# Performance work log

Measured on AMD Instinct MI355X. Metric: run time of the kernel, lower is better.

## Reference

```python
import jax, jax.numpy as jnp
import numpy as np

EPS = 1e-5
H = 8
N_BUCKETS = 32


def _instance_norm(x, gamma, beta):
    # x: [B, N, D]; torch InstanceNorm1d normalizes over the N (length) dim
    # per channel per batch element, using biased variance.
    m = jnp.mean(x, axis=1, keepdims=True)
    v = jnp.var(x, axis=1, keepdims=True)
    return (x - m) * jax.lax.rsqrt(v + EPS) * gamma + beta


def setup_inputs() -> dict:
    key = jax.random.key(0)
    ks = jax.random.split(key, 12)
    B, N, D, d_ff = 4, 512, 128, 512
    s = 1.0 / np.sqrt(D)
    sf = 1.0 / np.sqrt(d_ff)
    u = lambda k, shape, lim: jax.random.uniform(k, shape, jnp.float32, -lim, lim)
    return {
        "h": jax.random.normal(ks[0], (B, N, D), jnp.float32),
        "coords": jax.random.uniform(ks[1], (B, N, 2), jnp.float32),
        "W_Q": u(ks[2], (D, D), s),
        "W_K": u(ks[3], (D, D), s),
        "W_V": u(ks[4], (D, D), s),
        "W_O": u(ks[5], (D, D), s),
        "emb": jax.random.normal(ks[6], (N_BUCKETS, D), jnp.float32),  # n_heads*d_k == D
        "ffn_w1": u(ks[7], (D, d_ff), s),
        "ffn_b1": u(ks[8], (d_ff,), s),
        "ffn_w2": u(ks[9], (d_ff, D), sf),
        "ffn_b2": u(ks[10], (D,), sf),
        "gamma1": jnp.ones((D,), jnp.float32),
        "beta1": jnp.zeros((D,), jnp.float32),
        "gamma2": jnp.ones((D,), jnp.float32),
        "beta2": jnp.zeros((D,), jnp.float32),
    }


def reference(h, coords, W_Q, W_K, W_V, W_O, emb, ffn_w1, ffn_b1, ffn_w2,
              ffn_b2, gamma1, beta1, gamma2, beta2):
    B, N, D = h.shape
    Dk = D // H
    Q = (h @ W_Q).reshape(B, N, H, Dk)
    K = (h @ W_K).reshape(B, N, H, Dk)
    V = (h @ W_V).reshape(B, N, H, Dk)
    # content scores: [B, H, N, N]
    scores = jnp.einsum('bnhd,bmhd->bhnm', Q, K) / np.sqrt(Dk)
    # relative-distance bucket embeddings for all (i, j) pairs
    diff = coords[:, :, None, :] - coords[:, None, :, :]          # [B,N,N,2]
    dist = jax.lax.stop_gradient(jnp.sqrt(jnp.sum(diff * diff, -1)))
    buckets = jnp.clip((dist * N_BUCKETS).astype(jnp.int32), 0, N_BUCKETS - 1)
    r = emb[buckets].reshape(B, N, N, H, Dk)                      # [B,N,N,H,Dk]
    scores = scores + jnp.einsum('bnhd,bnmhd->bhnm', Q, r)
    attn = jax.nn.softmax(scores, axis=-1)
    h_attn = jnp.einsum('bhnm,bmhd->bnhd', attn, V).reshape(B, N, D) @ W_O
    h1 = _instance_norm(h + h_attn, gamma1, beta1)
    h_ffn = jax.nn.relu(h1 @ ffn_w1 + ffn_b1) @ ffn_w2 + ffn_b2
    return _instance_norm(h1 + h_ffn, gamma2, beta2)
```

## Files before the change

kernel.cpp:

```cpp
#include <hip/hip_runtime.h>
#include <hip/hip_bf16.h>

#define B_  4
#define N_  512
#define D_  128
#define H_  8
#define DK  16
#define DFF 512
#define NB  32
#define KS  4
#define FS  4

__global__ __launch_bounds__(256) void qkv_qe_kernel(
    const float* __restrict__ A,
    const float* __restrict__ WQ, const float* __restrict__ WK, const float* __restrict__ WV,
    const float* __restrict__ emb,
    float* __restrict__ Qo, float* __restrict__ Ko, float* __restrict__ Vo,
    float* __restrict__ QE)
{
    const float* Bw = blockIdx.z == 0 ? WQ : (blockIdx.z == 1 ? WK : WV);
    float*       C  = blockIdx.z == 0 ? Qo : (blockIdx.z == 1 ? Ko : Vo);
    const int wave = threadIdx.x >> 6;
    const int lane = threadIdx.x & 63;
    const int rbase = __builtin_amdgcn_readfirstlane((blockIdx.x * 4 + wave) * 2);
    const int col = lane * 2;

    float acc[2][2] = {};
#pragma unroll 2
    for (int k0 = 0; k0 < D_; k0 += 4) {
        float4 a0 = *(const float4*)&A[(size_t)(rbase + 0) * D_ + k0];
        float4 a1 = *(const float4*)&A[(size_t)(rbase + 1) * D_ + k0];
#pragma unroll
        for (int kk = 0; kk < 4; ++kk) {
            float2 bv = *(const float2*)&Bw[(size_t)(k0 + kk) * D_ + col];
            float x0 = (&a0.x)[kk], x1 = (&a1.x)[kk];
            acc[0][0] += x0 * bv.x; acc[0][1] += x0 * bv.y;
            acc[1][0] += x1 * bv.x; acc[1][1] += x1 * bv.y;
        }
    }
    *(float2*)&C[(size_t)(rbase + 0) * D_ + col] = make_float2(acc[0][0], acc[0][1]);
    *(float2*)&C[(size_t)(rbase + 1) * D_ + col] = make_float2(acc[1][0], acc[1][1]);

    if (blockIdx.z == 0) {
        __shared__ float Qls[8][132];
        *(float2*)&Qls[wave * 2 + 0][col] = make_float2(acc[0][0], acc[0][1]);
        *(float2*)&Qls[wave * 2 + 1][col] = make_float2(acc[1][0], acc[1][1]);
        __syncthreads();
        const int r  = threadIdx.x >> 5;
        const int hh = (threadIdx.x >> 2) & 7;
        const int k0 = (threadIdx.x & 3) * 8;
        const int grow = blockIdx.x * 8 + r;
        const float4* qv = (const float4*)&Qls[r][hh * DK];
        const float4 qa = qv[0], qb = qv[1], qc = qv[2], qd = qv[3];
        float* qe_out = QE + ((size_t)grow * H_ + hh) * NB + k0;
#pragma unroll 2
        for (int k = 0; k < 8; ++k) {
            const float4* ep = (const float4*)(emb + (size_t)(k0 + k) * D_ + hh * DK);
            float4 e0 = ep[0], e1 = ep[1], e2 = ep[2], e3 = ep[3];
            float d0 = fmaf(qa.x,e0.x, fmaf(qa.y,e0.y, fmaf(qa.z,e0.z, qa.w*e0.w)));
            float d1 = fmaf(qb.x,e1.x, fmaf(qb.y,e1.y, fmaf(qb.z,e1.z, qb.w*e1.w)));
            float d2 = fmaf(qc.x,e2.x, fmaf(qc.y,e2.y, fmaf(qc.z,e2.z, qc.w*e2.w)));
            float d3 = fmaf(qd.x,e3.x, fmaf(qd.y,e3.y, fmaf(qd.z,e3.z, qd.w*e3.w)));
            qe_out[k] = (d0 + d1) + (d2 + d3);
        }
    }
}

__global__ __launch_bounds__(256) void attn7_kernel(
    const float* __restrict__ Q, const float* __restrict__ K, const float* __restrict__ V,
    const float* __restrict__ QE, const float* __restrict__ coords,
    float* __restrict__ P)
{
    const int tid  = threadIdx.x;
    const int wave = tid >> 6;
    const int lane = tid & 63;
    const int bid  = blockIdx.x;
    const int ks    = bid & 3;
    const int chunk = (bid >> 2) & 7;
    const int h     = (bid >> 5) & (H_ - 1);
    const int b     = bid >> 8;
    const int row = b * N_ + chunk * 64 + lane;

    __shared__ float kl[64][16];
    __shared__ float vl[64][16];
    __shared__ float qel[64][NB + 1];
    __shared__ float ckrd[128][2];
    __shared__ float accl[4][64][17];

    const size_t hdbase = (size_t)b * N_ * D_ + h * DK;

    {
        int r = tid >> 2, part = tid & 3;
        const float* src = QE + ((size_t)(b * N_ + chunk * 64 + r) * H_ + h) * NB + part * 8;
#pragma unroll
        for (int j = 0; j < 8; ++j) qel[r][part * 8 + j] = src[j];
    }
    ((float*)ckrd)[tid] = coords[(size_t)(b * N_ + ks * 128) * 2 + tid];

    const float4* qp = (const float4*)(Q + (size_t)row * D_ + h * DK);
    const float4 q0 = qp[0], q1 = qp[1], q2 = qp[2], q3 = qp[3];
    const float cx = coords[(size_t)row * 2 + 0];
    const float cy = coords[(size_t)row * 2 + 1];

    float l = 0.f;
    float acc[16] = {};

    for (int rnd = 0; rnd < 2; ++rnd) {
        if (rnd) __syncthreads();
        {
            int key = tid >> 2, part = tid & 3;
            size_t g = hdbase + (size_t)(ks * 128 + rnd * 64 + key) * D_ + part * 4;
            *(float4*)&kl[key][part * 4] = *(const float4*)&K[g];
            *(float4*)&vl[key][part * 4] = *(const float4*)&V[g];
        }
        __syncthreads();

        const int ml0 = wave * 16;
#pragma unroll 4
        for (int i = 0; i < 16; ++i) {
            const int ml = ml0 + i;
            const int mc = rnd * 64 + ml;
            float dx = cx - ckrd[mc][0], dy = cy - ckrd[mc][1];
            float dist = sqrtf(fmaf(dx, dx, dy * dy));
            int bucket = (int)(dist * 32.0f);
            bucket = bucket > (NB - 1) ? (NB - 1) : bucket;
            float qe = qel[lane][bucket];
            const float4* kp = (const float4*)&kl[ml][0];
            const float4 k0 = kp[0], k1 = kp[1], k2 = kp[2], k3 = kp[3];
            float d0 = fmaf(q0.x,k0.x, fmaf(q0.y,k0.y, fmaf(q0.z,k0.z, q0.w*k0.w)));
            float d1 = fmaf(q1.x,k1.x, fmaf(q1.y,k1.y, fmaf(q1.z,k1.z, q1.w*k1.w)));
            float d2 = fmaf(q2.x,k2.x, fmaf(q2.y,k2.y, fmaf(q2.z,k2.z, q2.w*k2.w)));
            float d3 = fmaf(q3.x,k3.x, fmaf(q3.y,k3.y, fmaf(q3.z,k3.z, q3.w*k3.w)));
            float p = __expf(fmaf((d0 + d1) + (d2 + d3), 0.25f, qe));
            l += p;
            const float4* vp = (const float4*)&vl[ml][0];
            const float4 v0 = vp[0], v1 = vp[1], v2 = vp[2], v3 = vp[3];
            acc[0]  += p * v0.x; acc[1]  += p * v0.y; acc[2]  += p * v0.z; acc[3]  += p * v0.w;
            acc[4]  += p * v1.x; acc[5]  += p * v1.y; acc[6]  += p * v1.z; acc[7]  += p * v1.w;
            acc[8]  += p * v2.x; acc[9]  += p * v2.y; acc[10] += p * v2.z; acc[11] += p * v2.w;
            acc[12] += p * v3.x; acc[13] += p * v3.y; acc[14] += p * v3.z; acc[15] += p * v3.w;
        }
    }

    __syncthreads();
    accl[wave][lane][16] = l;
#pragma unroll
    for (int j = 0; j < 16; ++j) accl[wave][lane][j] = acc[j];
    __syncthreads();

    float* pb = P + (size_t)bid * (64 * 17);
    for (int i = tid; i < 64 * 17; i += 256) {
        int r = i / 17, j = i - r * 17;
        pb[i] = accl[0][r][j] + accl[1][r][j] + accl[2][r][j] + accl[3][r][j];
    }
}

__global__ __launch_bounds__(256) void oproj_kernel(
    const float* __restrict__ P, const float* __restrict__ WO,
    const float* __restrict__ hres, float* __restrict__ X1)
{
    const int tid = threadIdx.x;
    const int gr0 = blockIdx.x * 4;
    __shared__ float AOls[4][128];
    __shared__ float lsl[4][8];

    if (tid < 32) {
        int r = tid >> 3, hh = tid & 7;
        int gr = gr0 + r;
        int b = gr >> 9, n = gr & (N_ - 1);
        int chunk = n >> 6, rl = n & 63;
        size_t base = ((size_t)(((b * H_ + hh) * 8 + chunk) * KS)) * (64 * 17) + (size_t)rl * 17;
        float l = 0.f;
#pragma unroll
        for (int s = 0; s < KS; ++s) l += P[base + (size_t)s * (64 * 17) + 16];
        lsl[r][hh] = l;
    }
    float asum[2];
#pragma unroll
    for (int j = 0; j < 2; ++j) {
        int i = tid + j * 256;
        int r = i >> 7, d = i & 127;
        int gr = gr0 + r;
        int b = gr >> 9, n = gr & (N_ - 1);
        int chunk = n >> 6, rl = n & 63;
        int hh = d >> 4, dk = d & 15;
        size_t base = ((size_t)(((b * H_ + hh) * 8 + chunk) * KS)) * (64 * 17) + (size_t)rl * 17 + dk;
        float s = 0.f;
#pragma unroll
        for (int ss = 0; ss < KS; ++ss) s += P[base + (size_t)ss * (64 * 17)];
        asum[j] = s;
    }
    __syncthreads();
#pragma unroll
    for (int j = 0; j < 2; ++j) {
        int i = tid + j * 256;
        int r = i >> 7, d = i & 127;
        AOls[r][d] = asum[j] / lsl[r][d >> 4];
    }
    __syncthreads();

    const int wave = tid >> 6;
    const int lane = tid & 63;
    const int col = lane * 2;
    float acc0 = 0.f, acc1 = 0.f;
#pragma unroll 2
    for (int k0 = 0; k0 < D_; k0 += 4) {
        float4 av = *(const float4*)&AOls[wave][k0];
#pragma unroll
        for (int kk = 0; kk < 4; ++kk) {
            float2 bv = *(const float2*)&WO[(size_t)(k0 + kk) * D_ + col];
            float x = (&av.x)[kk];
            acc0 += x * bv.x; acc1 += x * bv.y;
        }
    }
    const int gr = gr0 + wave;
    float2 rv = *(const float2*)&hres[(size_t)gr * D_ + col];
    *(float2*)&X1[(size_t)gr * D_ + col] = make_float2(acc0 + rv.x, acc1 + rv.y);
}

__global__ __launch_bounds__(256) void stats_kernel(const float* __restrict__ X,
    const float* __restrict__ gamma, const float* __restrict__ beta,
    float* __restrict__ T1, float* __restrict__ T2)
{
    const int b  = blockIdx.x >> 5;
    const int dg = blockIdx.x & 31;
    const int dl = threadIdx.x & 3;
    const int nc = threadIdx.x >> 2;
    const float* xp = X + ((size_t)b * N_ + nc * 8) * D_ + dg * 4 + dl;
    float s = 0.f, q = 0.f;
#pragma unroll
    for (int i = 0; i < 8; ++i) { float x = xp[(size_t)i * D_]; s += x; q += x * x; }
    __shared__ float rs[64][4], rq[64][4];
    rs[nc][dl] = s; rq[nc][dl] = q;
    __syncthreads();
    for (int off = 32; off >= 1; off >>= 1) {
        if (nc < off) { rs[nc][dl] += rs[nc + off][dl]; rq[nc][dl] += rq[nc + off][dl]; }
        __syncthreads();
    }
    if (threadIdx.x < 4) {
        int d = dg * 4 + threadIdx.x;
        float mean = rs[0][threadIdx.x] * (1.0f / N_);
        float var  = rq[0][threadIdx.x] * (1.0f / N_) - mean * mean;
        float r = 1.0f / sqrtf(var + 1e-5f);
        float t1 = r * gamma[d];
        T1[b * D_ + d] = t1;
        T2[b * D_ + d] = beta[d] - mean * t1;
    }
}

__global__ __launch_bounds__(256) void ffn1_kernel(
    const float* __restrict__ X1, const float* __restrict__ T1, const float* __restrict__ T2,
    const float* __restrict__ w1, const float* __restrict__ b1, float* __restrict__ F1)
{
    __shared__ float Als[16][128];
    const int gr0 = blockIdx.x * 16;
    const int b = gr0 >> 9;
#pragma unroll
    for (int i = threadIdx.x * 4; i < 16 * 128; i += 1024) {
        int r = i >> 7, c = i & 127;
        float4 x  = *(const float4*)&X1[(size_t)(gr0 + r) * D_ + c];
        float4 t1 = *(const float4*)&T1[b * D_ + c];
        float4 t2 = *(const float4*)&T2[b * D_ + c];
        float4 y;
        y.x = x.x * t1.x + t2.x; y.y = x.y * t1.y + t2.y;
        y.z = x.z * t1.z + t2.z; y.w = x.w * t1.w + t2.w;
        *(float4*)&Als[r][c] = y;
    }
    __syncthreads();

    const int wave = threadIdx.x >> 6;
    const int lane = threadIdx.x & 63;
    const int rl = wave * 4;
    const int col = blockIdx.y * 128 + lane * 2;

    float acc[4][2] = {};
#pragma unroll 2
    for (int k0 = 0; k0 < D_; k0 += 4) {
        float4 a4[4];
#pragma unroll
        for (int j = 0; j < 4; ++j) a4[j] = *(const float4*)&Als[rl + j][k0];
#pragma unroll
        for (int kk = 0; kk < 4; ++kk) {
            float2 bv = *(const float2*)&w1[(size_t)(k0 + kk) * DFF + col];
#pragma unroll
            for (int j = 0; j < 4; ++j) {
                float x = (&a4[j].x)[kk];
                acc[j][0] += x * bv.x; acc[j][1] += x * bv.y;
            }
        }
    }
    float2 bb = *(const float2*)&b1[col];
#pragma unroll
    for (int j = 0; j < 4; ++j) {
        float o0 = fmaxf(acc[j][0] + bb.x, 0.f);
        float o1 = fmaxf(acc[j][1] + bb.y, 0.f);
        *(float2*)&F1[(size_t)(gr0 + rl + j) * DFF + col] = make_float2(o0, o1);
    }
}

__global__ __launch_bounds__(256) void ffn2s_kernel(
    const float* __restrict__ F1, const float* __restrict__ w2, float* __restrict__ Pf)
{
    const int wave = threadIdx.x >> 6;
    const int lane = threadIdx.x & 63;
    const int rbase = __builtin_amdgcn_readfirstlane((blockIdx.x * 4 + wave) * 4);
    const int col = lane * 2;
    const int s = blockIdx.z;
    const int kbeg = s * (DFF / FS);

    float acc[4][2] = {};
#pragma unroll 2
    for (int k0 = kbeg; k0 < kbeg + DFF / FS; k0 += 4) {
        float4 a4[4];
#pragma unroll
        for (int j = 0; j < 4; ++j)
            a4[j] = *(const float4*)&F1[(size_t)(rbase + j) * DFF + k0];
#pragma unroll
        for (int kk = 0; kk < 4; ++kk) {
            float2 bv = *(const float2*)&w2[(size_t)(k0 + kk) * D_ + col];
#pragma unroll
            for (int j = 0; j < 4; ++j) {
                float x = (&a4[j].x)[kk];
                acc[j][0] += x * bv.x; acc[j][1] += x * bv.y;
            }
        }
    }
#pragma unroll
    for (int j = 0; j < 4; ++j)
        *(float2*)&Pf[((size_t)s * (B_ * N_) + rbase + j) * D_ + col] =
            make_float2(acc[j][0], acc[j][1]);
}

__global__ __launch_bounds__(256) void fcomb_kernel(
    const float* __restrict__ Pf, const float* __restrict__ b2,
    const float* __restrict__ X1, const float* __restrict__ T1, const float* __restrict__ T2,
    float* __restrict__ X2)
{
    int idx = (blockIdx.x * 256 + threadIdx.x) * 4;
    int d = idx & (D_ - 1);
    int b = idx >> 16;
    float4 o  = *(const float4*)&b2[d];
    float4 x1 = *(const float4*)&X1[idx];
    float4 t1 = *(const float4*)&T1[b * D_ + d];
    float4 t2 = *(const float4*)&T2[b * D_ + d];
    o.x += x1.x * t1.x + t2.x; o.y += x1.y * t1.y + t2.y;
    o.z += x1.z * t1.z + t2.z; o.w += x1.w * t1.w + t2.w;
#pragma unroll
    for (int s = 0; s < FS; ++s) {
        float4 p = *(const float4*)&Pf[(size_t)s * (B_ * N_ * D_) + idx];
        o.x += p.x; o.y += p.y; o.z += p.z; o.w += p.w;
    }
    *(float4*)&X2[idx] = o;
}

__global__ __launch_bounds__(256) void stats_apply_kernel(const float* __restrict__ X,
    const float* __restrict__ gamma, const float* __restrict__ beta,
    float* __restrict__ Y)
{
    const int b  = blockIdx.x >> 5;
    const int dg = blockIdx.x & 31;
    const int dl = threadIdx.x & 3;
    const int nc = threadIdx.x >> 2;
    const float* xp = X + ((size_t)b * N_ + nc * 8) * D_ + dg * 4 + dl;
    float s = 0.f, q = 0.f;
#pragma unroll
    for (int i = 0; i < 8; ++i) { float x = xp[(size_t)i * D_]; s += x; q += x * x; }
    __shared__ float rs[64][4], rq[64][4];
    __shared__ float t1l[4], t2l[4];
    rs[nc][dl] = s; rq[nc][dl] = q;
    __syncthreads();
    for (int off = 32; off >= 1; off >>= 1) {
        if (nc < off) { rs[nc][dl] += rs[nc + off][dl]; rq[nc][dl] += rq[nc + off][dl]; }
        __syncthreads();
    }
    if (threadIdx.x < 4) {
        int d = dg * 4 + threadIdx.x;
        float mean = rs[0][threadIdx.x] * (1.0f / N_);
        float var  = rq[0][threadIdx.x] * (1.0f / N_) - mean * mean;
        float r = 1.0f / sqrtf(var + 1e-5f);
        float t1 = r * gamma[d];
        t1l[threadIdx.x] = t1;
        t2l[threadIdx.x] = beta[d] - mean * t1;
    }
    __syncthreads();
    const float t1 = t1l[dl], t2 = t2l[dl];
    float* yp = Y + ((size_t)b * N_ + nc * 8) * D_ + dg * 4 + dl;
#pragma unroll
    for (int i = 0; i < 8; ++i) yp[(size_t)i * D_] = xp[(size_t)i * D_] * t1 + t2;
}

extern "C" void kernel_launch(void* const* d_in, const int* in_sizes, int n_in,
                              void* d_out, int out_size, void* d_ws, size_t ws_size,
                              hipStream_t stream)
{
    const float* h      = (const float*)d_in[0];
    const float* coords = (const float*)d_in[1];
    const float* W_Q    = (const float*)d_in[2];
    const float* W_K    = (const float*)d_in[3];
    const float* W_V    = (const float*)d_in[4];
    const float* W_O    = (const float*)d_in[5];
    const float* emb    = (const float*)d_in[6];
    const float* w1     = (const float*)d_in[7];
    const float* b1     = (const float*)d_in[8];
    const float* w2     = (const float*)d_in[9];
    const float* b2     = (const float*)d_in[10];
    const float* g1     = (const float*)d_in[11];
    const float* be1    = (const float*)d_in[12];
    const float* g2     = (const float*)d_in[13];
    const float* be2    = (const float*)d_in[14];
    float* out = (float*)d_out;

    float* ws = (float*)d_ws;
    const size_t R = (size_t)B_ * N_;
    float* Qb  = ws;
    float* Kb  = Qb + R * D_;
    float* Vb  = Kb + R * D_;
    float* QEb = Vb + R * D_;
    float* X1  = QEb + R * H_ * NB;
    float* F1  = X1 + R * D_;
    float* X2  = F1 + R * DFF;
    float* Pb  = X2 + R * D_;
    float* Pf  = Pb + (size_t)1024 * 64 * 17;
    float* T1a = Pf + (size_t)FS * R * D_;
    float* T2a = T1a + B_ * D_;

    qkv_qe_kernel<<<dim3(256, 1, 3), 256, 0, stream>>>(
        h, W_Q, W_K, W_V, emb, Qb, Kb, Vb, QEb);
    attn7_kernel<<<dim3(1024), 256, 0, stream>>>(Qb, Kb, Vb, QEb, coords, Pb);
    oproj_kernel<<<dim3((int)R / 4), 256, 0, stream>>>(Pb, W_O, h, X1);
    stats_kernel<<<dim3(B_ * 32), 256, 0, stream>>>(X1, g1, be1, T1a, T2a);
    ffn1_kernel<<<dim3(128, 4), 256, 0, stream>>>(X1, T1a, T2a, w1, b1, F1);
    ffn2s_kernel<<<dim3(128, 1, FS), 256, 0, stream>>>(F1, w2, Pf);
    fcomb_kernel<<<dim3((int)(R * D_) / 1024), 256, 0, stream>>>(Pf, b2, X1, T1a, T2a, X2);
    stats_apply_kernel<<<dim3(B_ * 32), 256, 0, stream>>>(X2, g2, be2, out);
}
```

Measured before the change: 86.20 us.

## Drop attention key split and fuse norm stats with both FFN GEMMs

The attention kernel now processes all 512 keys per block instead of splitting them four ways. It normalizes and writes the attention output directly, so the output projection no longer reduces partial sums. The instance-norm stats, both FFN GEMMs and the residual combine are fused into one kernel, with the intermediate kept in shared memory. This cuts kernel launches and intermediate global traffic. In exchange, attention runs only 256 blocks, which lowers parallelism and occupancy, and every FFN block redundantly recomputes the per-batch norm statistics.

```diff
diff --git a/kernel.cpp b/kernel.cpp
--- a/kernel.cpp
+++ b/kernel.cpp
@@ -8,8 +8,6 @@
 #define DK  16
 #define DFF 512
 #define NB  32
-#define KS  4
-#define FS  4
 
 __global__ __launch_bounds__(256) void qkv_qe_kernel(
     const float* __restrict__ A,
@@ -66,25 +64,24 @@
     }
 }
 
-__global__ __launch_bounds__(256) void attn7_kernel(
+__global__ __launch_bounds__(256) void attn8_kernel(
     const float* __restrict__ Q, const float* __restrict__ K, const float* __restrict__ V,
     const float* __restrict__ QE, const float* __restrict__ coords,
-    float* __restrict__ P)
+    float* __restrict__ AO)
 {
     const int tid  = threadIdx.x;
     const int wave = tid >> 6;
     const int lane = tid & 63;
     const int bid  = blockIdx.x;
-    const int ks    = bid & 3;
-    const int chunk = (bid >> 2) & 7;
-    const int h     = (bid >> 5) & (H_ - 1);
-    const int b     = bid >> 8;
+    const int chunk = bid & 7;
+    const int h     = (bid >> 3) & 7;
+    const int b     = bid >> 6;
     const int row = b * N_ + chunk * 64 + lane;
 
-    __shared__ float kl[64][16];
-    __shared__ float vl[64][16];
+    __shared__ float kl[256][16];
+    __shared__ float vl[256][16];
     __shared__ float qel[64][NB + 1];
-    __shared__ float ckrd[128][2];
+    __shared__ float ckrd[512][2];
     __shared__ float accl[4][64][17];
 
     const size_t hdbase = (size_t)b * N_ * D_ + h * DK;
@@ -95,7 +92,9 @@
 #pragma unroll
         for (int j = 0; j < 8; ++j) qel[r][part * 8 + j] = src[j];
     }
-    ((float*)ckrd)[tid] = coords[(size_t)(b * N_ + ks * 128) * 2 + tid];
+#pragma unroll
+    for (int j = 0; j < 4; ++j)
+        ((float*)ckrd)[tid + j * 256] = coords[(size_t)(b * N_) * 2 + tid + j * 256];
 
     const float4* qp = (const float4*)(Q + (size_t)row * D_ + h * DK);
     const float4 q0 = qp[0], q1 = qp[1], q2 = qp[2], q3 = qp[3];
@@ -108,18 +107,22 @@
     for (int rnd = 0; rnd < 2; ++rnd) {
         if (rnd) __syncthreads();
         {
-            int key = tid >> 2, part = tid & 3;
-            size_t g = hdbase + (size_t)(ks * 128 + rnd * 64 + key) * D_ + part * 4;
-            *(float4*)&kl[key][part * 4] = *(const float4*)&K[g];
-            *(float4*)&vl[key][part * 4] = *(const float4*)&V[g];
+            int part = tid & 3, kb = tid >> 2;
+#pragma unroll
+            for (int j = 0; j < 4; ++j) {
+                int key = j * 64 + kb;
+                size_t g = hdbase + (size_t)(rnd * 256 + key) * D_ + part * 4;
+                *(float4*)&kl[key][part * 4] = *(const float4*)&K[g];
+                *(float4*)&vl[key][part * 4] = *(const float4*)&V[g];
+            }
         }
         __syncthreads();
 
-        const int ml0 = wave * 16;
+        const int ml0 = wave * 64;
 #pragma unroll 4
-        for (int i = 0; i < 16; ++i) {
+        for (int i = 0; i < 64; ++i) {
             const int ml = ml0 + i;
-            const int mc = rnd * 64 + ml;
+            const int mc = rnd * 256 + ml;
             float dx = cx - ckrd[mc][0], dy = cy - ckrd[mc][1];
             float dist = sqrtf(fmaf(dx, dx, dy * dy));
             int bucket = (int)(dist * 32.0f);
@@ -148,64 +151,29 @@
     for (int j = 0; j < 16; ++j) accl[wave][lane][j] = acc[j];
     __syncthreads();
 
-    float* pb = P + (size_t)bid * (64 * 17);
-    for (int i = tid; i < 64 * 17; i += 256) {
-        int r = i / 17, j = i - r * 17;
-        pb[i] = accl[0][r][j] + accl[1][r][j] + accl[2][r][j] + accl[3][r][j];
+#pragma unroll
+    for (int j = 0; j < 4; ++j) {
+        int i = tid + j * 256;
+        int r = i >> 4, dk = i & 15;
+        float num = accl[0][r][dk] + accl[1][r][dk] + accl[2][r][dk] + accl[3][r][dk];
+        float den = accl[0][r][16] + accl[1][r][16] + accl[2][r][16] + accl[3][r][16];
+        AO[(size_t)(b * N_ + chunk * 64 + r) * D_ + h * DK + dk] = num / den;
     }
 }
 
 __global__ __launch_bounds__(256) void oproj_kernel(
-    const float* __restrict__ P, const float* __restrict__ WO,
+    const float* __restrict__ AO, const float* __restrict__ WO,
     const float* __restrict__ hres, float* __restrict__ X1)
 {
-    const int tid = threadIdx.x;
-    const int gr0 = blockIdx.x * 4;
-    __shared__ float AOls[4][128];
-    __shared__ float lsl[4][8];
-
-    if (tid < 32) {
-        int r = tid >> 3, hh = tid & 7;
-        int gr = gr0 + r;
-        int b = gr >> 9, n = gr & (N_ - 1);
-        int chunk = n >> 6, rl = n & 63;
-        size_t base = ((size_t)(((b * H_ + hh) * 8 + chunk) * KS)) * (64 * 17) + (size_t)rl * 17;
-        float l = 0.f;
-#pragma unroll
-        for (int s = 0; s < KS; ++s) l += P[base + (size_t)s * (64 * 17) + 16];
-        lsl[r][hh] = l;
-    }
-    float asum[2];
-#pragma unroll
-    for (int j = 0; j < 2; ++j) {
-        int i = tid + j * 256;
-        int r = i >> 7, d = i & 127;
-        int gr = gr0 + r;
-        int b = gr >> 9, n = gr & (N_ - 1);
-        int chunk = n >> 6, rl = n & 63;
-        int hh = d >> 4, dk = d & 15;
-        size_t base = ((size_t)(((b * H_ + hh) * 8 + chunk) * KS)) * (64 * 17) + (size_t)rl * 17 + dk;
-        float s = 0.f;
-#pragma unroll
-        for (int ss = 0; ss < KS; ++ss) s += P[base + (size_t)ss * (64 * 17)];
-        asum[j] = s;
-    }
-    __syncthreads();
-#pragma unroll
-    for (int j = 0; j < 2; ++j) {
-        int i = tid + j * 256;
-        int r = i >> 7, d = i & 127;
-        AOls[r][d] = asum[j] / lsl[r][d >> 4];
-    }
-    __syncthreads();
-
-    const int wave = tid >> 6;
-    const int lane = tid & 63;
+    const int wave = threadIdx.x >> 6;
+    const int lane = threadIdx.x & 63;
+    const int gr = __builtin_amdgcn_readfirstlane(blockIdx.x * 4 + wave);
     const int col = lane * 2;
+
     float acc0 = 0.f, acc1 = 0.f;
 #pragma unroll 2
     for (int k0 = 0; k0 < D_; k0 += 4) {
-        float4 av = *(const float4*)&AOls[wave][k0];
+        float4 av = *(const float4*)&AO[(size_t)gr * D_ + k0];
 #pragma unroll
         for (int kk = 0; kk < 4; ++kk) {
             float2 bv = *(const float2*)&WO[(size_t)(k0 + kk) * D_ + col];
@@ -213,144 +181,130 @@
             acc0 += x * bv.x; acc1 += x * bv.y;
         }
     }
-    const int gr = gr0 + wave;
     float2 rv = *(const float2*)&hres[(size_t)gr * D_ + col];
     *(float2*)&X1[(size_t)gr * D_ + col] = make_float2(acc0 + rv.x, acc1 + rv.y);
 }
 
-__global__ __launch_bounds__(256) void stats_kernel(const float* __restrict__ X,
-    const float* __restrict__ gamma, const float* __restrict__ beta,
-    float* __restrict__ T1, float* __restrict__ T2)
-{
-    const int b  = blockIdx.x >> 5;
-    const int dg = blockIdx.x & 31;
-    const int dl = threadIdx.x & 3;
-    const int nc = threadIdx.x >> 2;
-    const float* xp = X + ((size_t)b * N_ + nc * 8) * D_ + dg * 4 + dl;
-    float s = 0.f, q = 0.f;
-#pragma unroll
-    for (int i = 0; i < 8; ++i) { float x = xp[(size_t)i * D_]; s += x; q += x * x; }
-    __shared__ float rs[64][4], rq[64][4];
-    rs[nc][dl] = s; rq[nc][dl] = q;
-    __syncthreads();
-    for (int off = 32; off >= 1; off >>= 1) {
-        if (nc < off) { rs[nc][dl] += rs[nc + off][dl]; rq[nc][dl] += rq[nc + off][dl]; }
-        __syncthreads();
-    }
-    if (threadIdx.x < 4) {
-        int d = dg * 4 + threadIdx.x;
-        float mean = rs[0][threadIdx.x] * (1.0f / N_);
-        float var  = rq[0][threadIdx.x] * (1.0f / N_) - mean * mean;
+__global__ __launch_bounds__(256) void ffn_kernel(
+    const float* __restrict__ X1,
+    const float* __restrict__ g1, const float* __restrict__ be1,
+    const float* __restrict__ w1, const float* __restrict__ b1,
+    const float* __restrict__ w2, const float* __restrict__ b2,
+    float* __restrict__ X2)
+{
+    const int tid = threadIdx.x;
+    const int wave = tid >> 6;
+    const int lane = tid & 63;
+    const int gr0 = blockIdx.x * 8;
+    const int b = gr0 >> 9;
+
+    __shared__ float rs[8][128], rq[8][128];
+    __shared__ float t1l[128], t2l[128];
+    __shared__ float Als[8][128];
+    __shared__ float F1ls[8][DFF];
+
+    {
+        int d4 = (tid & 31) * 4, seg = tid >> 5;
+        const float* xp = X1 + ((size_t)(b * N_ + seg * 64)) * D_ + d4;
+        float4 s4 = make_float4(0.f,0.f,0.f,0.f), q4 = s4;
+#pragma unroll 4
+        for (int i = 0; i < 64; ++i) {
+            float4 x = *(const float4*)&xp[(size_t)i * D_];
+            s4.x += x.x; s4.y += x.y; s4.z += x.z; s4.w += x.w;
+            q4.x += x.x*x.x; q4.y += x.y*x.y; q4.z += x.z*x.z; q4.w += x.w*x.w;
+        }
+        *(float4*)&rs[seg][d4] = s4;
+        *(float4*)&rq[seg][d4] = q4;
+    }
+    __syncthreads();
+    if (tid < 128) {
+        float S = 0.f, Q2 = 0.f;
+#pragma unroll
+        for (int s = 0; s < 8; ++s) { S += rs[s][tid]; Q2 += rq[s][tid]; }
+        float mean = S * (1.0f / N_);
+        float var  = Q2 * (1.0f / N_) - mean * mean;
         float r = 1.0f / sqrtf(var + 1e-5f);
-        float t1 = r * gamma[d];
-        T1[b * D_ + d] = t1;
-        T2[b * D_ + d] = beta[d] - mean * t1;
-    }
-}
-
-__global__ __launch_bounds__(256) void ffn1_kernel(
-    const float* __restrict__ X1, const float* __restrict__ T1, const float* __restrict__ T2,
-    const float* __restrict__ w1, const float* __restrict__ b1, float* __restrict__ F1)
-{
-    __shared__ float Als[16][128];
-    const int gr0 = blockIdx.x * 16;
-    const int b = gr0 >> 9;
-#pragma unroll
-    for (int i = threadIdx.x * 4; i < 16 * 128; i += 1024) {
+        float t1 = r * g1[tid];
+        t1l[tid] = t1;
+        t2l[tid] = be1[tid] - mean * t1;
+    }
+    __syncthreads();
+
+    {
+        int i = tid * 4;
         int r = i >> 7, c = i & 127;
         float4 x  = *(const float4*)&X1[(size_t)(gr0 + r) * D_ + c];
-        float4 t1 = *(const float4*)&T1[b * D_ + c];
-        float4 t2 = *(const float4*)&T2[b * D_ + c];
         float4 y;
-        y.x = x.x * t1.x + t2.x; y.y = x.y * t1.y + t2.y;
-        y.z = x.z * t1.z + t2.z; y.w = x.w * t1.w + t2.w;
+        y.x = x.x * t1l[c+0] + t2l[c+0]; y.y = x.y * t1l[c+1] + t2l[c+1];
+        y.z = x.z * t1l[c+2] + t2l[c+2]; y.w = x.w * t1l[c+3] + t2l[c+3];
         *(float4*)&Als[r][c] = y;
     }
     __syncthreads();
 
-    const int wave = threadIdx.x >> 6;
-    const int lane = threadIdx.x & 63;
-    const int rl = wave * 4;
-    const int col = blockIdx.y * 128 + lane * 2;
-
-    float acc[4][2] = {};
+    const int r0 = wave * 2;
+    const int c1 = lane * 8;
+    float acc1[2][8] = {};
 #pragma unroll 2
     for (int k0 = 0; k0 < D_; k0 += 4) {
-        float4 a4[4];
-#pragma unroll
-        for (int j = 0; j < 4; ++j) a4[j] = *(const float4*)&Als[rl + j][k0];
+        float4 a0 = *(const float4*)&Als[r0 + 0][k0];
+        float4 a1 = *(const float4*)&Als[r0 + 1][k0];
 #pragma unroll
         for (int kk = 0; kk < 4; ++kk) {
-            float2 bv = *(const float2*)&w1[(size_t)(k0 + kk) * DFF + col];
-#pragma unroll
-            for (int j = 0; j < 4; ++j) {
-                float x = (&a4[j].x)[kk];
-                acc[j][0] += x * bv.x; acc[j][1] += x * bv.y;
-            }
-        }
-    }
-    float2 bb = *(const float2*)&b1[col];
-#pragma unroll
-    for (int j = 0; j < 4; ++j) {
-        float o0 = fmaxf(acc[j][0] + bb.x, 0.f);
-        float o1 = fmaxf(acc[j][1] + bb.y, 0.f);
-        *(float2*)&F1[(size_t)(gr0 + rl + j) * DFF + col] = make_float2(o0, o1);
-    }
-}
-
-__global__ __launch_bounds__(256) void ffn2s_kernel(
-    const float* __restrict__ F1, const float* __restrict__ w2, float* __restrict__ Pf)
-{
-    const int wave = threadIdx.x >> 6;
-    const int lane = threadIdx.x & 63;
-    const int rbase = __builtin_amdgcn_readfirstlane((blockIdx.x * 4 + wave) * 4);
-    const int col = lane * 2;
-    const int s = blockIdx.z;
-    const int kbeg = s * (DFF / FS);
-
-    float acc[4][2] = {};
-#pragma unroll 2
-    for (int k0 = kbeg; k0 < kbeg + DFF / FS; k0 += 4) {
-        float4 a4[4];
-#pragma unroll
-        for (int j = 0; j < 4; ++j)
-            a4[j] = *(const float4*)&F1[(size_t)(rbase + j) * DFF + k0];
+            float4 b0 = *(const float4*)&w1[(size_t)(k0 + kk) * DFF + c1];
+            float4 b4 = *(const float4*)&w1[(size_t)(k0 + kk) * DFF + c1 + 4];
+            float x0 = (&a0.x)[kk], x1 = (&a1.x)[kk];
+            acc1[0][0] += x0 * b0.x; acc1[0][1] += x0 * b0.y;
+            acc1[0][2] += x0 * b0.z; acc1[0][3] += x0 * b0.w;
+            acc1[0][4] += x0 * b4.x; acc1[0][5] += x0 * b4.y;
+            acc1[0][6] += x0 * b4.z; acc1[0][7] += x0 * b4.w;
+            acc1[1][0] += x1 * b0.x; acc1[1][1] += x1 * b0.y;
+            acc1[1][2] += x1 * b0.z; acc1[1][3] += x1 * b0.w;
+            acc1[1][4] += x1 * b4.x; acc1[1][5] += x1 * b4.y;
+            acc1[1][6] += x1 * b4.z; acc1[1][7] += x1 * b4.w;
+        }
+    }
+    {
+        float4 bb0 = *(const float4*)&b1[c1];
+        float4 bb4 = *(const float4*)&b1[c1 + 4];
+#pragma unroll
+        for (int j = 0; j < 2; ++j) {
+            float4 o0, o4;
+            o0.x = fmaxf(acc1[j][0] + bb0.x, 0.f); o0.y = fmaxf(acc1[j][1] + bb0.y, 0.f);
+            o0.z = fmaxf(acc1[j][2] + bb0.z, 0.f); o0.w = fmaxf(acc1[j][3] + bb0.w, 0.f);
+            o4.x = fmaxf(acc1[j][4] + bb4.x, 0.f); o4.y = fmaxf(acc1[j][5] + bb4.y, 0.f);
+            o4.z = fmaxf(acc1[j][6] + bb4.z, 0.f); o4.w = fmaxf(acc1[j][7] + bb4.w, 0.f);
+            *(float4*)&F1ls[r0 + j][c1]     = o0;
+            *(float4*)&F1ls[r0 + j][c1 + 4] = o4;
+        }
+    }
+
+    const int c2 = lane * 2;
+    float acc2[2][2] = {};
+#pragma unroll 2
+    for (int k0 = 0; k0 < DFF; k0 += 4) {
+        float4 f0 = *(const float4*)&F1ls[r0 + 0][k0];
+        float4 f1 = *(const float4*)&F1ls[r0 + 1][k0];
 #pragma unroll
         for (int kk = 0; kk < 4; ++kk) {
-            float2 bv = *(const float2*)&w2[(size_t)(k0 + kk) * D_ + col];
-#pragma unroll
-            for (int j = 0; j < 4; ++j) {
-                float x = (&a4[j].x)[kk];
-                acc[j][0] += x * bv.x; acc[j][1] += x * bv.y;
-            }
-        }
-    }
-#pragma unroll
-    for (int j = 0; j < 4; ++j)
-        *(float2*)&Pf[((size_t)s * (B_ * N_) + rbase + j) * D_ + col] =
-            make_float2(acc[j][0], acc[j][1]);
-}
-
-__global__ __launch_bounds__(256) void fcomb_kernel(
-    const float* __restrict__ Pf, const float* __restrict__ b2,
-    const float* __restrict__ X1, const float* __restrict__ T1, const float* __restrict__ T2,
-    float* __restrict__ X2)
-{
-    int idx = (blockIdx.x * 256 + threadIdx.x) * 4;
-    int d = idx & (D_ - 1);
-    int b = idx >> 16;
-    float4 o  = *(const float4*)&b2[d];
-    float4 x1 = *(const float4*)&X1[idx];
-    float4 t1 = *(const float4*)&T1[b * D_ + d];
-    float4 t2 = *(const float4*)&T2[b * D_ + d];
-    o.x += x1.x * t1.x + t2.x; o.y += x1.y * t1.y + t2.y;
-    o.z += x1.z * t1.z + t2.z; o.w += x1.w * t1.w + t2.w;
-#pragma unroll
-    for (int s = 0; s < FS; ++s) {
-        float4 p = *(const float4*)&Pf[(size_t)s * (B_ * N_ * D_) + idx];
-        o.x += p.x; o.y += p.y; o.z += p.z; o.w += p.w;
-    }
-    *(float4*)&X2[idx] = o;
+            float2 bv = *(const float2*)&w2[(size_t)(k0 + kk) * D_ + c2];
+            float x0 = (&f0.x)[kk], x1 = (&f1.x)[kk];
+            acc2[0][0] += x0 * bv.x; acc2[0][1] += x0 * bv.y;
+            acc2[1][0] += x1 * bv.x; acc2[1][1] += x1 * bv.y;
+        }
+    }
+    {
+        float2 bb = *(const float2*)&b2[c2];
+        float t1a = t1l[c2], t1b = t1l[c2 + 1];
+        float t2a = t2l[c2], t2b = t2l[c2 + 1];
+#pragma unroll
+        for (int j = 0; j < 2; ++j) {
+            int row = gr0 + r0 + j;
+            float2 x1v = *(const float2*)&X1[(size_t)row * D_ + c2];
+            float o0 = acc2[j][0] + bb.x + (x1v.x * t1a + t2a);
+            float o1 = acc2[j][1] + bb.y + (x1v.y * t1b + t2b);
+            *(float2*)&X2[(size_t)row * D_ + c2] = make_float2(o0, o1);
+        }
+    }
 }
 
 __global__ __launch_bounds__(256) void stats_apply_kernel(const float* __restrict__ X,
@@ -416,21 +370,14 @@
     float* Kb  = Qb + R * D_;
     float* Vb  = Kb + R * D_;
     float* QEb = Vb + R * D_;
-    float* X1  = QEb + R * H_ * NB;
-    float* F1  = X1 + R * D_;
-    float* X2  = F1 + R * DFF;
-    float* Pb  = X2 + R * D_;
-    float* Pf  = Pb + (size_t)1024 * 64 * 17;
-    float* T1a = Pf + (size_t)FS * R * D_;
-    float* T2a = T1a + B_ * D_;
+    float* AO  = QEb + R * H_ * NB;
+    float* X1  = AO + R * D_;
+    float* X2  = X1 + R * D_;
 
     qkv_qe_kernel<<<dim3(256, 1, 3), 256, 0, stream>>>(
         h, W_Q, W_K, W_V, emb, Qb, Kb, Vb, QEb);
-    attn7_kernel<<<dim3(1024), 256, 0, stream>>>(Qb, Kb, Vb, QEb, coords, Pb);
-    oproj_kernel<<<dim3((int)R / 4), 256, 0, stream>>>(Pb, W_O, h, X1);
-    stats_kernel<<<dim3(B_ * 32), 256, 0, stream>>>(X1, g1, be1, T1a, T2a);
-    ffn1_kernel<<<dim3(128, 4), 256, 0, stream>>>(X1, T1a, T2a, w1, b1, F1);
-    ffn2s_kernel<<<dim3(128, 1, FS), 256, 0, stream>>>(F1, w2, Pf);
-    fcomb_kernel<<<dim3((int)(R * D_) / 1024), 256, 0, stream>>>(Pf, b2, X1, T1a, T2a, X2);
+    attn8_kernel<<<dim3(256), 256, 0, stream>>>(Qb, Kb, Vb, QEb, coords, AO);
+    oproj_kernel<<<dim3((int)R / 4), 256, 0, stream>>>(AO, W_O, h, X1);
+    ffn_kernel<<<dim3((int)R / 8), 256, 0, stream>>>(X1, g1, be1, w1, b1, w2, b2, X2);
     stats_apply_kernel<<<dim3(B_ * 32), 256, 0, stream>>>(X2, g2, be2, out);
 }
```

After: 101.7 us. +17.9%, slower.
